# Kernel tuning notes

Hardware: AMD Instinct MI355X
Metric: run time of the kernel (lower is better)

The kernel has to match this reference:

```python
import jax, jax.numpy as jnp
import numpy as np

NUM_PIECE_TYPES = 7
NUM_COLORS = 3
NUM_CASTLING_STATES = 16
NUM_EP_STATES = 9
D = 256
B = 4096
EPS = 1e-5


def setup_inputs() -> dict:
    key = jax.random.key(0)
    ks = jax.random.split(key, 12)
    inp = {
        'piece_ids': jax.random.randint(ks[0], (B, 64), 0, NUM_PIECE_TYPES),
        'color_ids': jax.random.randint(ks[1], (B, 64), 0, NUM_COLORS),
        'turn': jax.random.randint(ks[2], (B,), 0, 2),
        'castling': jax.random.randint(ks[3], (B,), 0, NUM_CASTLING_STATES),
        'ep_file': jax.random.randint(ks[4], (B,), 0, NUM_EP_STATES),
        # learned parameters
        'piece_table': jax.random.normal(ks[5], (NUM_PIECE_TYPES, D), jnp.float32) * 0.02,
        'W': jax.random.normal(ks[6], (NUM_COLORS, D, D), jnp.float32) * (1.0 / np.sqrt(D)),
        'b': jax.random.normal(ks[7], (NUM_COLORS, D), jnp.float32) * 0.02,
        'square_table': jax.random.normal(ks[8], (64, D), jnp.float32) * 0.02,
        'turn_table': jax.random.normal(ks[9], (2, D), jnp.float32) * 0.02,
        'castling_table': jax.random.normal(ks[10], (NUM_CASTLING_STATES, D), jnp.float32) * 0.02,
        'ep_table': jax.random.normal(ks[11], (NUM_EP_STATES, D), jnp.float32) * 0.02,
        'gamma': jnp.ones((D,), jnp.float32),
        'beta': jnp.zeros((D,), jnp.float32),
    }
    return inp


def _layernorm(x, gamma, beta):
    mu = jnp.mean(x, axis=-1, keepdims=True)
    var = jnp.mean(jnp.square(x - mu), axis=-1, keepdims=True)
    return (x - mu) * jax.lax.rsqrt(var + EPS) * gamma + beta


def reference(piece_ids, color_ids, turn, castling, ep_file,
              piece_table, W, b, square_table, turn_table,
              castling_table, ep_table, gamma, beta):
    piece_emb = piece_table[piece_ids]                      # (B,64,D)
    # per-color linear: proj_stack[b,s,c] = piece_emb[b,s] @ W[c].T + b[c]
    proj_stack = jnp.einsum('bsd,cod->bsco', piece_emb, W) + b  # (B,64,C,D)
    # select the projection for each square's color (== one-hot mask + sum)
    idx = color_ids[..., None, None]                        # (B,64,1,1)
    sq_emb = jnp.take_along_axis(proj_stack, idx, axis=2)[:, :, 0, :]  # (B,64,D)
    sq_emb = sq_emb + square_table[None, :, :]              # add positional
    turn_tok = turn_table[turn][:, None, :]                 # (B,1,D)
    castle_tok = castling_table[castling][:, None, :]       # (B,1,D)
    ep_tok = ep_table[ep_file][:, None, :]                  # (B,1,D)
    tokens = jnp.concatenate([turn_tok, castle_tok, ep_tok, sq_emb], axis=1)  # (B,67,D)
    return _layernorm(tokens, gamma, beta)
```

## Files before the change

### kernel.cpp

```cpp
#include <hip/hip_runtime.h>


#define DIM 256
#define NPT 7
#define NCOL 3
#define NROWS_SQ (NPT * NCOL * 64)
#define ROW_TURN 1344
#define ROW_CASTLE 1346
#define ROW_EP 1362
#define NROWS_TOT 1371
#define EPSV 1e-5f

typedef float f32x4 __attribute__((ext_vector_type(4)));

__global__ void proj_kernel(const float* __restrict__ piece_table,
                            const float* __restrict__ W,
                            const float* __restrict__ bvec,
                            float* __restrict__ proj) {
    int e = blockIdx.x;
    int p = e / NCOL, c = e % NCOL;
    int d = threadIdx.x;
    __shared__ float pt[DIM];
    pt[d] = piece_table[p * DIM + d];
    __syncthreads();
    const float4* w4 = (const float4*)(W + (size_t)c * DIM * DIM + (size_t)d * DIM);
    float acc = bvec[c * DIM + d];
    #pragma unroll 8
    for (int k = 0; k < DIM / 4; ++k) {
        float4 w = w4[k];
        acc += w.x * pt[k * 4 + 0] + w.y * pt[k * 4 + 1]
             + w.z * pt[k * 4 + 2] + w.w * pt[k * 4 + 3];
    }
    proj[e * DIM + d] = acc;
}

__global__ void ln_table_kernel(const float* __restrict__ proj,
                                const float* __restrict__ square_table,
                                const float* __restrict__ turn_table,
                                const float* __restrict__ castling_table,
                                const float* __restrict__ ep_table,
                                const float* __restrict__ gamma,
                                const float* __restrict__ beta,
                                float* __restrict__ table) {
    int w = blockIdx.x * 4 + (threadIdx.x >> 6);
    int lane = threadIdx.x & 63;
    if (w >= NROWS_TOT) return;

    float4 x;
    if (w < NROWS_SQ) {
        int p = w / 192;
        int rem = w - p * 192;
        int c = rem >> 6;
        int s = rem & 63;
        float4 a = ((const float4*)(proj + (p * NCOL + c) * DIM))[lane];
        float4 q = ((const float4*)(square_table + s * DIM))[lane];
        x = make_float4(a.x + q.x, a.y + q.y, a.z + q.z, a.w + q.w);
    } else if (w < ROW_CASTLE) {
        x = ((const float4*)(turn_table + (w - ROW_TURN) * DIM))[lane];
    } else if (w < ROW_EP) {
        x = ((const float4*)(castling_table + (w - ROW_CASTLE) * DIM))[lane];
    } else {
        x = ((const float4*)(ep_table + (w - ROW_EP) * DIM))[lane];
    }

    float s = x.x + x.y + x.z + x.w;
    #pragma unroll
    for (int m = 1; m < 64; m <<= 1) s += __shfl_xor(s, m, 64);
    float mu = s * (1.0f / DIM);

    float dx = x.x - mu, dy = x.y - mu, dz = x.z - mu, dw = x.w - mu;
    float v = dx * dx + dy * dy + dz * dz + dw * dw;
    #pragma unroll
    for (int m = 1; m < 64; m <<= 1) v += __shfl_xor(v, m, 64);
    float inv = rsqrtf(v * (1.0f / DIM) + EPSV);

    float4 g = ((const float4*)gamma)[lane];
    float4 bb = ((const float4*)beta)[lane];
    float4 y = make_float4(dx * inv * g.x + bb.x,
                           dy * inv * g.y + bb.y,
                           dz * inv * g.z + bb.z,
                           dw * inv * g.w + bb.w);
    ((float4*)(table + (size_t)w * DIM))[lane] = y;
}

__global__ __launch_bounds__(256) void gather_kernel(
        const int* __restrict__ piece_ids,
        const int* __restrict__ color_ids,
        const int* __restrict__ turn,
        const int* __restrict__ castling,
        const int* __restrict__ ep_file,
        const float* __restrict__ table,
        float* __restrict__ out) {
    int b = blockIdx.x;
    __shared__ int rows[67];
    int tid = threadIdx.x;
    if (tid < 64) {
        int pid = piece_ids[b * 64 + tid];
        int cid = color_ids[b * 64 + tid];
        rows[3 + tid] = pid * (NCOL * 64) + cid * 64 + tid;
    } else if (tid == 64) {
        rows[0] = ROW_TURN + turn[b];
    } else if (tid == 65) {
        rows[1] = ROW_CASTLE + castling[b];
    } else if (tid == 66) {
        rows[2] = ROW_EP + ep_file[b];
    }
    __syncthreads();

    int wave = tid >> 6, lane = tid & 63;
    f32x4* outb = (f32x4*)(out + (size_t)b * 67 * DIM);
    #pragma unroll 4
    for (int t = wave; t < 67; t += 4) {
        f32x4 v = ((const f32x4*)(table + (size_t)rows[t] * DIM))[lane];
        __builtin_nontemporal_store(v, outb + t * (DIM / 4) + lane);
    }
}

extern "C" void kernel_launch(void* const* d_in, const int* in_sizes, int n_in,
                              void* d_out, int out_size, void* d_ws, size_t ws_size,
                              hipStream_t stream) {
    const int*   piece_ids      = (const int*)d_in[0];
    const int*   color_ids      = (const int*)d_in[1];
    const int*   turn           = (const int*)d_in[2];
    const int*   castling       = (const int*)d_in[3];
    const int*   ep_file        = (const int*)d_in[4];
    const float* piece_table    = (const float*)d_in[5];
    const float* W              = (const float*)d_in[6];
    const float* bvec           = (const float*)d_in[7];
    const float* square_table   = (const float*)d_in[8];
    const float* turn_table     = (const float*)d_in[9];
    const float* castling_table = (const float*)d_in[10];
    const float* ep_table       = (const float*)d_in[11];
    const float* gamma          = (const float*)d_in[12];
    const float* beta           = (const float*)d_in[13];
    float* out = (float*)d_out;

    int B = in_sizes[0] / 64;

    float* proj  = (float*)d_ws;
    float* table = proj + NPT * NCOL * DIM;

    proj_kernel<<<NPT * NCOL, 256, 0, stream>>>(piece_table, W, bvec, proj);
    ln_table_kernel<<<(NROWS_TOT + 3) / 4, 256, 0, stream>>>(
        proj, square_table, turn_table, castling_table, ep_table, gamma, beta, table);
    gather_kernel<<<B, 256, 0, stream>>>(
        piece_ids, color_ids, turn, castling, ep_file, table, out);
}
```

Before: 70.42 us.

## Fuse projection and layernorm table build into one kernel; use plain stores

Merges the per-(piece,color) projection kernel and the layernorm table kernel into a single launch with 22 blocks. Each block computes its projection into shared memory, then layernorms the 64 square rows for that pair; one extra block handles the turn, castling and en-passant rows. This removes one kernel launch and the global round-trip of the projection, at the cost of much lower parallelism in the table build (22 blocks instead of ~343). The gather kernel also switches from nontemporal stores to ordinary stores for the output.

```diff
diff --git a/kernel.cpp b/kernel.cpp
--- a/kernel.cpp
+++ b/kernel.cpp
@@ -11,76 +11,76 @@
 #define NROWS_TOT 1371
 #define EPSV 1e-5f
 
-typedef float f32x4 __attribute__((ext_vector_type(4)));
-
-__global__ void proj_kernel(const float* __restrict__ piece_table,
-                            const float* __restrict__ W,
-                            const float* __restrict__ bvec,
-                            float* __restrict__ proj) {
-    int e = blockIdx.x;
-    int p = e / NCOL, c = e % NCOL;
-    int d = threadIdx.x;
-    __shared__ float pt[DIM];
-    pt[d] = piece_table[p * DIM + d];
-    __syncthreads();
-    const float4* w4 = (const float4*)(W + (size_t)c * DIM * DIM + (size_t)d * DIM);
-    float acc = bvec[c * DIM + d];
-    #pragma unroll 8
-    for (int k = 0; k < DIM / 4; ++k) {
-        float4 w = w4[k];
-        acc += w.x * pt[k * 4 + 0] + w.y * pt[k * 4 + 1]
-             + w.z * pt[k * 4 + 2] + w.w * pt[k * 4 + 3];
-    }
-    proj[e * DIM + d] = acc;
-}
-
-__global__ void ln_table_kernel(const float* __restrict__ proj,
-                                const float* __restrict__ square_table,
-                                const float* __restrict__ turn_table,
-                                const float* __restrict__ castling_table,
-                                const float* __restrict__ ep_table,
-                                const float* __restrict__ gamma,
-                                const float* __restrict__ beta,
-                                float* __restrict__ table) {
-    int w = blockIdx.x * 4 + (threadIdx.x >> 6);
-    int lane = threadIdx.x & 63;
-    if (w >= NROWS_TOT) return;
-
-    float4 x;
-    if (w < NROWS_SQ) {
-        int p = w / 192;
-        int rem = w - p * 192;
-        int c = rem >> 6;
-        int s = rem & 63;
-        float4 a = ((const float4*)(proj + (p * NCOL + c) * DIM))[lane];
-        float4 q = ((const float4*)(square_table + s * DIM))[lane];
-        x = make_float4(a.x + q.x, a.y + q.y, a.z + q.z, a.w + q.w);
-    } else if (w < ROW_CASTLE) {
-        x = ((const float4*)(turn_table + (w - ROW_TURN) * DIM))[lane];
-    } else if (w < ROW_EP) {
-        x = ((const float4*)(castling_table + (w - ROW_CASTLE) * DIM))[lane];
-    } else {
-        x = ((const float4*)(ep_table + (w - ROW_EP) * DIM))[lane];
-    }
-
+__device__ __forceinline__ float4 ln4(float4 x, float4 g, float4 bb) {
     float s = x.x + x.y + x.z + x.w;
     #pragma unroll
     for (int m = 1; m < 64; m <<= 1) s += __shfl_xor(s, m, 64);
     float mu = s * (1.0f / DIM);
-
     float dx = x.x - mu, dy = x.y - mu, dz = x.z - mu, dw = x.w - mu;
     float v = dx * dx + dy * dy + dz * dz + dw * dw;
     #pragma unroll
     for (int m = 1; m < 64; m <<= 1) v += __shfl_xor(v, m, 64);
     float inv = rsqrtf(v * (1.0f / DIM) + EPSV);
+    return make_float4(dx * inv * g.x + bb.x,
+                       dy * inv * g.y + bb.y,
+                       dz * inv * g.z + bb.z,
+                       dw * inv * g.w + bb.w);
+}
 
-    float4 g = ((const float4*)gamma)[lane];
+__global__ __launch_bounds__(256) void table_kernel(
+        const float* __restrict__ piece_table,
+        const float* __restrict__ W,
+        const float* __restrict__ bvec,
+        const float* __restrict__ square_table,
+        const float* __restrict__ turn_table,
+        const float* __restrict__ castling_table,
+        const float* __restrict__ ep_table,
+        const float* __restrict__ gamma,
+        const float* __restrict__ beta,
+        float* __restrict__ table) {
+    int e = blockIdx.x;
+    int tid = threadIdx.x;
+    int wave = tid >> 6, lane = tid & 63;
+    float4 g  = ((const float4*)gamma)[lane];
     float4 bb = ((const float4*)beta)[lane];
-    float4 y = make_float4(dx * inv * g.x + bb.x,
-                           dy * inv * g.y + bb.y,
-                           dz * inv * g.z + bb.z,
-                           dw * inv * g.w + bb.w);
-    ((float4*)(table + (size_t)w * DIM))[lane] = y;
+
+    if (e < NPT * NCOL) {
+        int p = e / NCOL, c = e % NCOL;
+        __shared__ float pt[DIM];
+        __shared__ float projs[DIM];
+        pt[tid] = piece_table[p * DIM + tid];
+        __syncthreads();
+        const float4* w4 = (const float4*)(W + (size_t)c * DIM * DIM + (size_t)tid * DIM);
+        float acc = bvec[c * DIM + tid];
+        #pragma unroll 8
+        for (int k = 0; k < DIM / 4; ++k) {
+            float4 w = w4[k];
+            acc += w.x * pt[k * 4 + 0] + w.y * pt[k * 4 + 1]
+                 + w.z * pt[k * 4 + 2] + w.w * pt[k * 4 + 3];
+        }
+        projs[tid] = acc;
+        __syncthreads();
+
+        float4 a = ((const float4*)projs)[lane];
+        float* tbase = table + (size_t)(p * (NCOL * 64) + c * 64) * DIM;
+        for (int s = wave; s < 64; s += 4) {
+            float4 q = ((const float4*)(square_table + s * DIM))[lane];
+            float4 x = make_float4(a.x + q.x, a.y + q.y, a.z + q.z, a.w + q.w);
+            ((float4*)(tbase + (size_t)s * DIM))[lane] = ln4(x, g, bb);
+        }
+    } else {
+        for (int w = wave; w < 27; w += 4) {
+            float4 x;
+            if (w < 2) {
+                x = ((const float4*)(turn_table + w * DIM))[lane];
+            } else if (w < 18) {
+                x = ((const float4*)(castling_table + (w - 2) * DIM))[lane];
+            } else {
+                x = ((const float4*)(ep_table + (w - 18) * DIM))[lane];
+            }
+            ((float4*)(table + (size_t)(ROW_TURN + w) * DIM))[lane] = ln4(x, g, bb);
+        }
+    }
 }
 
 __global__ __launch_bounds__(256) void gather_kernel(
@@ -108,11 +108,11 @@
     __syncthreads();
 
     int wave = tid >> 6, lane = tid & 63;
-    f32x4* outb = (f32x4*)(out + (size_t)b * 67 * DIM);
+    float4* outb = (float4*)(out + (size_t)b * 67 * DIM);
     #pragma unroll 4
     for (int t = wave; t < 67; t += 4) {
-        f32x4 v = ((const f32x4*)(table + (size_t)rows[t] * DIM))[lane];
-        __builtin_nontemporal_store(v, outb + t * (DIM / 4) + lane);
+        float4 v = ((const float4*)(table + (size_t)rows[t] * DIM))[lane];
+        outb[t * (DIM / 4) + lane] = v;
     }
 }
 
@@ -136,13 +136,11 @@
     float* out = (float*)d_out;
 
     int B = in_sizes[0] / 64;
+    float* table = (float*)d_ws;
 
-    float* proj  = (float*)d_ws;
-    float* table = proj + NPT * NCOL * DIM;
-
-    proj_kernel<<<NPT * NCOL, 256, 0, stream>>>(piece_table, W, bvec, proj);
-    ln_table_kernel<<<(NROWS_TOT + 3) / 4, 256, 0, stream>>>(
-        proj, square_table, turn_table, castling_table, ep_table, gamma, beta, table);
+    table_kernel<<<NPT * NCOL + 1, 256, 0, stream>>>(
+        piece_table, W, bvec, square_table, turn_table, castling_table,
+        ep_table, gamma, beta, table);
     gather_kernel<<<B, 256, 0, stream>>>(
         piece_ids, color_ids, turn, castling, ep_file, table, out);
 }
```

Result: slower. 74.73 us (+6.1%).
